# Kernel tuning notes

Measured on AMD Instinct MI355X. Metric: run time of the kernel, lower is better.

The kernel has to match this reference:

```python
import jax, jax.numpy as jnp
import numpy as np

NUM_NODES = 200000
EMB_DIM = 64
NUM_EDGES = 6400000
NUM_LAYERS = 4


def setup_inputs() -> dict:
    key = jax.random.key(0)
    k1, k2, k3, k4 = jax.random.split(key, 4)
    embeds = jax.random.normal(k1, (NUM_NODES, EMB_DIM), dtype=jnp.float32)
    adj_rows = jax.random.randint(k2, (NUM_EDGES,), 0, NUM_NODES, dtype=jnp.int64)
    adj_cols = jax.random.randint(k3, (NUM_EDGES,), 0, NUM_NODES, dtype=jnp.int64)
    adj_vals = jax.random.uniform(k4, (NUM_EDGES,), dtype=jnp.float32)
    return {"embeds": embeds, "adj_rows": adj_rows, "adj_cols": adj_cols, "adj_vals": adj_vals}


def _spmm(rows, cols, vals, x):
    # Sparse (COO) adjacency @ dense x: out[r] += v * x[c]
    msgs = vals[:, None] * x[cols]  # [E, d] gather + scale
    return jax.ops.segment_sum(msgs, rows, num_segments=NUM_NODES)


def reference(embeds, adj_rows, adj_cols, adj_vals):
    x = embeds
    acc = x  # running sum over layer outputs (fuses stack+mean)
    for _ in range(NUM_LAYERS):
        x = _spmm(adj_rows, adj_cols, adj_vals, x)
        acc = acc + x
    return acc / jnp.float32(NUM_LAYERS + 1)
```

## Files before the change

### kernel.cpp

```cpp
#include <hip/hip_runtime.h>

#define N_NODES 200000
#define DIM 64
#define BSHIFT 8
#define BROWS 256
#define NB 782
#define NB_PAD 1024
#define CHUNK 4096
#define NS 8
#define NBINS 2048

__device__ __forceinline__ unsigned short f2bf(float f) {
    unsigned int u = __float_as_uint(f);
    u += 0x7FFFu + ((u >> 16) & 1u);
    return (unsigned short)(u >> 16);
}
__device__ __forceinline__ int stripe_of(int c) { return (int)((unsigned)c / 25000u); }

__global__ __launch_bounds__(256) void bucket_hist(const int* __restrict__ rows, int E,
                                                   int* __restrict__ bcnt) {
    __shared__ int h[NB_PAD];
    for (int i = threadIdx.x; i < NB_PAD; i += 256) h[i] = 0;
    __syncthreads();
    int stride = gridDim.x * blockDim.x;
    for (int e = blockIdx.x * blockDim.x + threadIdx.x; e < E; e += stride)
        atomicAdd(&h[rows[e] >> BSHIFT], 1);
    __syncthreads();
    for (int i = threadIdx.x; i < NB; i += 256)
        if (h[i]) atomicAdd(&bcnt[i], h[i]);
}

__global__ __launch_bounds__(1024) void bucket_scan(const int* __restrict__ bcnt,
                                                    int* __restrict__ bbase,
                                                    int* __restrict__ bcur) {
    __shared__ int wsum[16];
    int t = threadIdx.x;
    int v = (t < NB) ? bcnt[t] : 0;
    int incl = v;
    for (int off = 1; off < 64; off <<= 1) {
        int u = __shfl_up(incl, off);
        if ((t & 63) >= off) incl += u;
    }
    if ((t & 63) == 63) wsum[t >> 6] = incl;
    __syncthreads();
    if (t < 16) {
        int w = wsum[t];
        for (int off = 1; off < 16; off <<= 1) {
            int u = __shfl_up(w, off);
            if (t >= off) w += u;
        }
        wsum[t] = w;
    }
    __syncthreads();
    int wb = (t >= 64) ? wsum[(t >> 6) - 1] : 0;
    int excl = wb + incl - v;
    if (t < NB) { bbase[t] = excl; bcur[t] = excl; }
    if (t == NB - 1) bbase[NB] = excl + v;
}

__global__ __launch_bounds__(512) void bucket_scatter(const int* __restrict__ rows,
                                                      const int* __restrict__ cols,
                                                      const float* __restrict__ vals, int E,
                                                      int* __restrict__ bcur,
                                                      int2* __restrict__ tmp) {
    __shared__ int h[NB_PAD];
    __shared__ int cur2[NB_PAD];
    __shared__ int wtot[8];
    __shared__ int2 stage[CHUNK];
    __shared__ unsigned short sbkt[CHUNK];
    const int base = blockIdx.x * CHUNK;
    const int count = min(CHUNK, E - base);
    const int t = threadIdx.x;

    for (int i = t; i < NB_PAD; i += 512) h[i] = 0;
    __syncthreads();

    int myr[8], myc[8];
    float myv[8];
#pragma unroll
    for (int k = 0; k < 8; ++k) {
        int i = t + k * 512;
        if (i < count) {
            myr[k] = rows[base + i];
            myc[k] = cols[base + i];
            myv[k] = vals[base + i];
            atomicAdd(&h[myr[k] >> BSHIFT], 1);
        }
    }
    __syncthreads();

    int h0 = h[2 * t], h1 = h[2 * t + 1];
    int s = h0 + h1;
    int incl = s;
    for (int off = 1; off < 64; off <<= 1) {
        int u = __shfl_up(incl, off);
        if ((t & 63) >= off) incl += u;
    }
    if ((t & 63) == 63) wtot[t >> 6] = incl;
    __syncthreads();
    int wb = 0;
    for (int w = 0; w < (t >> 6); ++w) wb += wtot[w];
    int excl = wb + incl - s;
    cur2[2 * t] = excl;
    cur2[2 * t + 1] = excl + h0;
    __syncthreads();

    for (int i = t; i < NB; i += 512) {
        int hi = h[i];
        int g = hi ? atomicAdd(&bcur[i], hi) : 0;
        h[i] = g - cur2[i];
    }
    __syncthreads();

#pragma unroll
    for (int k = 0; k < 8; ++k) {
        int i = t + k * 512;
        if (i < count) {
            int r = myr[k];
            int b = r >> BSHIFT;
            int slot = atomicAdd(&cur2[b], 1);
            stage[slot] = make_int2(((r & (BROWS - 1)) << 18) | myc[k], __float_as_int(myv[k]));
            sbkt[slot] = (unsigned short)b;
        }
    }
    __syncthreads();
    for (int s2 = t; s2 < count; s2 += 512)
        tmp[s2 + h[sbkt[s2]]] = stage[s2];
}

__global__ __launch_bounds__(512) void bucket_sort(const int2* __restrict__ tmp,
                                                   const int* __restrict__ bbase,
                                                   int2* __restrict__ sorted,
                                                   int* __restrict__ row_start) {
    __shared__ int h[NBINS];
    __shared__ int wtot[8];
    const int bk = blockIdx.x;
    const int s0 = bbase[bk], s1 = bbase[bk + 1];
    const int t = threadIdx.x;
#pragma unroll
    for (int k = 0; k < NBINS / 512; ++k) h[t + k * 512] = 0;
    __syncthreads();
    for (int e = s0 + t; e < s1; e += 512) {
        int key = tmp[e].x;
        int bin = ((key >> 18) << 3) | stripe_of(key & 0x3FFFF);
        atomicAdd(&h[bin], 1);
    }
    __syncthreads();
    int b[4], ssum = 0;
#pragma unroll
    for (int k = 0; k < 4; ++k) { b[k] = h[4 * t + k]; ssum += b[k]; }
    int incl = ssum;
    for (int off = 1; off < 64; off <<= 1) {
        int u = __shfl_up(incl, off);
        if ((t & 63) >= off) incl += u;
    }
    if ((t & 63) == 63) wtot[t >> 6] = incl;
    __syncthreads();
    int wb = 0;
    for (int w = 0; w < (t >> 6); ++w) wb += wtot[w];
    int run = wb + incl - ssum;
    int rbase = bk << BSHIFT;
#pragma unroll
    for (int k = 0; k < 4; ++k) {
        int bin = 4 * t + k;
        h[bin] = run;
        if ((bin & 7) == 0) {
            int row = rbase + (bin >> 3);
            if (row < N_NODES) row_start[row] = s0 + run;
        }
        run += b[k];
    }
    if (bk == NB - 1 && t == 0) row_start[N_NODES] = s1;
    __syncthreads();
    for (int e = s0 + t; e < s1; e += 512) {
        int2 kv = tmp[e];
        int c = kv.x & 0x3FFFF;
        int bin = ((kv.x >> 18) << 3) | stripe_of(c);
        int rank = atomicAdd(&h[bin], 1);
        sorted[s0 + rank] = make_int2(c, kv.y);
    }
}

__global__ __launch_bounds__(256) void convert_kernel(const float* __restrict__ src,
                                                      unsigned short* __restrict__ dst, int n4) {
    int i = blockIdx.x * blockDim.x + threadIdx.x;
    if (i >= n4) return;
    float4 v = *(const float4*)(src + i * 4);
    ushort4 o;
    o.x = f2bf(v.x); o.y = f2bf(v.y); o.z = f2bf(v.z); o.w = f2bf(v.w);
    *(ushort4*)(dst + i * 4) = o;
}

#define BF_LO(u) __uint_as_float((u) << 16)
#define BF_HI(u) __uint_as_float((u) & 0xFFFF0000u)
#define FMA8(G, V)                              \
    do {                                        \
        a0 = fmaf((V), BF_LO((G).x), a0);       \
        a1 = fmaf((V), BF_HI((G).x), a1);       \
        a2 = fmaf((V), BF_LO((G).y), a2);       \
        a3 = fmaf((V), BF_HI((G).y), a3);       \
        a4 = fmaf((V), BF_LO((G).z), a4);       \
        a5 = fmaf((V), BF_HI((G).z), a5);       \
        a6 = fmaf((V), BF_LO((G).w), a6);       \
        a7 = fmaf((V), BF_HI((G).w), a7);       \
    } while (0)

template <int MODE>
__global__ __launch_bounds__(256) void spmm_kernel(const int2* __restrict__ sorted,
                                                   const int* __restrict__ row_start,
                                                   const unsigned short* __restrict__ xb,
                                                   const float* __restrict__ embeds,
                                                   unsigned short* __restrict__ y,
                                                   float* __restrict__ acc) {
    int gid = blockIdx.x * blockDim.x + threadIdx.x;
    int r = gid >> 3;
    if (r >= N_NODES) return;
    int j = (gid & 7) << 3;
    const unsigned short* xbj = xb + j;
    int e = row_start[r], eend = row_start[r + 1];
    float a0 = 0.f, a1 = 0.f, a2 = 0.f, a3 = 0.f, a4 = 0.f, a5 = 0.f, a6 = 0.f, a7 = 0.f;

    int2 c0 = make_int2(0, 0), c1 = make_int2(0, 0);
    int2 c2 = make_int2(0, 0), c3 = make_int2(0, 0);
    if (e + 4 <= eend) {
        c0 = sorted[e]; c1 = sorted[e + 1]; c2 = sorted[e + 2]; c3 = sorted[e + 3];
    }
    while (e + 8 <= eend) {
        uint4 g0 = *(const uint4*)(xbj + (c0.x << 6));
        uint4 g1 = *(const uint4*)(xbj + (c1.x << 6));
        uint4 g2 = *(const uint4*)(xbj + (c2.x << 6));
        uint4 g3 = *(const uint4*)(xbj + (c3.x << 6));
        int2 n0 = sorted[e + 4], n1 = sorted[e + 5];
        int2 n2 = sorted[e + 6], n3 = sorted[e + 7];
        float v0 = __int_as_float(c0.y), v1 = __int_as_float(c1.y);
        float v2 = __int_as_float(c2.y), v3 = __int_as_float(c3.y);
        FMA8(g0, v0); FMA8(g1, v1); FMA8(g2, v2); FMA8(g3, v3);
        c0 = n0; c1 = n1; c2 = n2; c3 = n3;
        e += 4;
    }
    if (e + 4 <= eend) {
        uint4 g0 = *(const uint4*)(xbj + (c0.x << 6));
        uint4 g1 = *(const uint4*)(xbj + (c1.x << 6));
        uint4 g2 = *(const uint4*)(xbj + (c2.x << 6));
        uint4 g3 = *(const uint4*)(xbj + (c3.x << 6));
        float v0 = __int_as_float(c0.y), v1 = __int_as_float(c1.y);
        float v2 = __int_as_float(c2.y), v3 = __int_as_float(c3.y);
        FMA8(g0, v0); FMA8(g1, v1); FMA8(g2, v2); FMA8(g3, v3);
        e += 4;
    }
    for (; e < eend; ++e) {
        int2 cv = sorted[e];
        uint4 g = *(const uint4*)(xbj + (cv.x << 6));
        float v = __int_as_float(cv.y);
        FMA8(g, v);
    }

    int o = (r << 6) + j;
    if (MODE == 0) {
        uint4 yo;
        yo.x = (unsigned)f2bf(a0) | ((unsigned)f2bf(a1) << 16);
        yo.y = (unsigned)f2bf(a2) | ((unsigned)f2bf(a3) << 16);
        yo.z = (unsigned)f2bf(a4) | ((unsigned)f2bf(a5) << 16);
        yo.w = (unsigned)f2bf(a6) | ((unsigned)f2bf(a7) << 16);
        *(uint4*)(y + o) = yo;
        float4 x0 = *(const float4*)(embeds + o);
        float4 x1 = *(const float4*)(embeds + o + 4);
        *(float4*)(acc + o)     = make_float4(x0.x + a0, x0.y + a1, x0.z + a2, x0.w + a3);
        *(float4*)(acc + o + 4) = make_float4(x1.x + a4, x1.y + a5, x1.z + a6, x1.w + a7);
    } else if (MODE == 1) {
        uint4 yo;
        yo.x = (unsigned)f2bf(a0) | ((unsigned)f2bf(a1) << 16);
        yo.y = (unsigned)f2bf(a2) | ((unsigned)f2bf(a3) << 16);
        yo.z = (unsigned)f2bf(a4) | ((unsigned)f2bf(a5) << 16);
        yo.w = (unsigned)f2bf(a6) | ((unsigned)f2bf(a7) << 16);
        *(uint4*)(y + o) = yo;
        float4 q0 = *(const float4*)(acc + o);
        float4 q1 = *(const float4*)(acc + o + 4);
        *(float4*)(acc + o)     = make_float4(q0.x + a0, q0.y + a1, q0.z + a2, q0.w + a3);
        *(float4*)(acc + o + 4) = make_float4(q1.x + a4, q1.y + a5, q1.z + a6, q1.w + a7);
    } else {
        const float sc = 0.2f;
        float4 q0 = *(const float4*)(acc + o);
        float4 q1 = *(const float4*)(acc + o + 4);
        *(float4*)(acc + o)     = make_float4((q0.x + a0) * sc, (q0.y + a1) * sc,
                                              (q0.z + a2) * sc, (q0.w + a3) * sc);
        *(float4*)(acc + o + 4) = make_float4((q1.x + a4) * sc, (q1.y + a5) * sc,
                                              (q1.z + a6) * sc, (q1.w + a7) * sc);
    }
}

extern "C" void kernel_launch(void* const* d_in, const int* in_sizes, int n_in,
                              void* d_out, int out_size, void* d_ws, size_t ws_size,
                              hipStream_t stream) {
    const float* embeds = (const float*)d_in[0];
    const int*   rows   = (const int*)d_in[1];
    const int*   cols   = (const int*)d_in[2];
    const float* vals   = (const float*)d_in[3];
    float* acc = (float*)d_out;
    const int E = in_sizes[1];

    char* ws = (char*)d_ws;
    size_t off = 0;
    auto alloc = [&](size_t bytes) -> char* {
        char* p = ws + off;
        off = (off + bytes + 255) & ~(size_t)255;
        return p;
    };
    int*   bcnt      = (int*)alloc((size_t)NB * 4);
    int*   bbase     = (int*)alloc((size_t)(NB + 1) * 4);
    int*   bcur      = (int*)alloc((size_t)NB * 4);
    int*   row_start = (int*)alloc((size_t)(N_NODES + 1) * 4);
    int2*  sorted    = (int2*)alloc((size_t)E * 8);
    unsigned short* xb0 = (unsigned short*)alloc((size_t)N_NODES * DIM * 2);
    unsigned short* xb1 = (unsigned short*)alloc((size_t)N_NODES * DIM * 2);
    int2*  tmp       = (int2*)alloc((size_t)E * 8);

    hipMemsetAsync(bcnt, 0, (size_t)NB * 4, stream);

    bucket_hist<<<1024, 256, 0, stream>>>(rows, E, bcnt);
    bucket_scan<<<1, 1024, 0, stream>>>(bcnt, bbase, bcur);
    bucket_scatter<<<(E + CHUNK - 1) / CHUNK, 512, 0, stream>>>(rows, cols, vals, E, bcur, tmp);
    bucket_sort<<<NB, 512, 0, stream>>>(tmp, bbase, sorted, row_start);

    int n4 = N_NODES * DIM / 4;
    convert_kernel<<<(n4 + 255) / 256, 256, 0, stream>>>(embeds, xb0, n4);

    int sb = (N_NODES * 8 + 255) / 256;
    spmm_kernel<0><<<sb, 256, 0, stream>>>(sorted, row_start, xb0, embeds, xb1, acc);
    spmm_kernel<1><<<sb, 256, 0, stream>>>(sorted, row_start, xb1, embeds, xb0, acc);
    spmm_kernel<1><<<sb, 256, 0, stream>>>(sorted, row_start, xb0, embeds, xb1, acc);
    spmm_kernel<2><<<sb, 256, 0, stream>>>(sorted, row_start, xb1, embeds, xb0, acc);
}
```

Before: 850.8 us.

## Stripe-ordered per-bucket SpMM with deferred layer merge kernel

The bucket sort now orders edges stripe-major within each 256-row bucket and writes per-stripe row offsets. The SpMM becomes one block per bucket that walks the column stripes in turn, with each thread accumulating 8 rows, so gathered x rows are reused while a stripe is hot in cache. The per-layer fp32 accumulator read-modify-write is replaced by keeping all four layer outputs in bf16 and combining them in a single final merge kernel. The cost is far fewer, register-heavy threads with only two gathers in flight each, which may hurt latency hiding. The edge stream is read with nontemporal loads, and the temp sort buffer is reused as storage for two layer outputs.

```diff
diff --git a/kernel.cpp b/kernel.cpp
--- a/kernel.cpp
+++ b/kernel.cpp
@@ -9,7 +9,11 @@
 #define CHUNK 4096
 #define NS 8
 #define NBINS 2048
-
+#define RS2_PITCH 257
+
+__device__ __forceinline__ float bf2f(unsigned short u) {
+    return __uint_as_float(((unsigned int)u) << 16);
+}
 __device__ __forceinline__ unsigned short f2bf(float f) {
     unsigned int u = __float_as_uint(f);
     u += 0x7FFFu + ((u >> 16) & 1u);
@@ -131,7 +135,7 @@
 __global__ __launch_bounds__(512) void bucket_sort(const int2* __restrict__ tmp,
                                                    const int* __restrict__ bbase,
                                                    int2* __restrict__ sorted,
-                                                   int* __restrict__ row_start) {
+                                                   int* __restrict__ rs2) {
     __shared__ int h[NBINS];
     __shared__ int wtot[8];
     const int bk = blockIdx.x;
@@ -142,7 +146,7 @@
     __syncthreads();
     for (int e = s0 + t; e < s1; e += 512) {
         int key = tmp[e].x;
-        int bin = ((key >> 18) << 3) | stripe_of(key & 0x3FFFF);
+        int bin = (stripe_of(key & 0x3FFFF) << 8) | (key >> 18);
         atomicAdd(&h[bin], 1);
     }
     __syncthreads();
@@ -159,23 +163,22 @@
     int wb = 0;
     for (int w = 0; w < (t >> 6); ++w) wb += wtot[w];
     int run = wb + incl - ssum;
-    int rbase = bk << BSHIFT;
-#pragma unroll
-    for (int k = 0; k < 4; ++k) {
-        int bin = 4 * t + k;
-        h[bin] = run;
-        if ((bin & 7) == 0) {
-            int row = rbase + (bin >> 3);
-            if (row < N_NODES) row_start[row] = s0 + run;
-        }
-        run += b[k];
-    }
-    if (bk == NB - 1 && t == 0) row_start[N_NODES] = s1;
+#pragma unroll
+    for (int k = 0; k < 4; ++k) { h[4 * t + k] = run; run += b[k]; }
+    __syncthreads();
+    for (int i = t; i < NS * RS2_PITCH; i += 512) {
+        int s = i / RS2_PITCH;
+        int rl = i - s * RS2_PITCH;
+        int val;
+        if (rl < 256) val = s0 + h[(s << 8) + rl];
+        else          val = (s < NS - 1) ? s0 + h[(s + 1) << 8] : s1;
+        rs2[((size_t)s * NB + bk) * RS2_PITCH + rl] = val;
+    }
     __syncthreads();
     for (int e = s0 + t; e < s1; e += 512) {
         int2 kv = tmp[e];
         int c = kv.x & 0x3FFFF;
-        int bin = ((kv.x >> 18) << 3) | stripe_of(c);
+        int bin = (stripe_of(c) << 8) | (kv.x >> 18);
         int rank = atomicAdd(&h[bin], 1);
         sorted[s0 + rank] = make_int2(c, kv.y);
     }
@@ -193,100 +196,110 @@
 
 #define BF_LO(u) __uint_as_float((u) << 16)
 #define BF_HI(u) __uint_as_float((u) & 0xFFFF0000u)
-#define FMA8(G, V)                              \
+#define FMA8A(A, G, V)                          \
     do {                                        \
-        a0 = fmaf((V), BF_LO((G).x), a0);       \
-        a1 = fmaf((V), BF_HI((G).x), a1);       \
-        a2 = fmaf((V), BF_LO((G).y), a2);       \
-        a3 = fmaf((V), BF_HI((G).y), a3);       \
-        a4 = fmaf((V), BF_LO((G).z), a4);       \
-        a5 = fmaf((V), BF_HI((G).z), a5);       \
-        a6 = fmaf((V), BF_LO((G).w), a6);       \
-        a7 = fmaf((V), BF_HI((G).w), a7);       \
+        A[0] = fmaf((V), BF_LO((G).x), A[0]);   \
+        A[1] = fmaf((V), BF_HI((G).x), A[1]);   \
+        A[2] = fmaf((V), BF_LO((G).y), A[2]);   \
+        A[3] = fmaf((V), BF_HI((G).y), A[3]);   \
+        A[4] = fmaf((V), BF_LO((G).z), A[4]);   \
+        A[5] = fmaf((V), BF_HI((G).z), A[5]);   \
+        A[6] = fmaf((V), BF_LO((G).w), A[6]);   \
+        A[7] = fmaf((V), BF_HI((G).w), A[7]);   \
     } while (0)
 
-template <int MODE>
-__global__ __launch_bounds__(256) void spmm_kernel(const int2* __restrict__ sorted,
-                                                   const int* __restrict__ row_start,
-                                                   const unsigned short* __restrict__ xb,
-                                                   const float* __restrict__ embeds,
-                                                   unsigned short* __restrict__ y,
-                                                   float* __restrict__ acc) {
-    int gid = blockIdx.x * blockDim.x + threadIdx.x;
-    int r = gid >> 3;
-    if (r >= N_NODES) return;
-    int j = (gid & 7) << 3;
+__global__ __launch_bounds__(256, 4) void spmm_kernel(const int2* __restrict__ sorted,
+                                                      const int* __restrict__ rs2,
+                                                      const unsigned short* __restrict__ xb,
+                                                      unsigned short* __restrict__ y) {
+    __shared__ int rsl[NS * RS2_PITCH];
+    const int bk = blockIdx.x;
+    const int t = threadIdx.x;
+    for (int i = t; i < NS * RS2_PITCH; i += 256) {
+        int s = i / RS2_PITCH;
+        rsl[i] = rs2[((size_t)s * NB + bk) * RS2_PITCH + (i - s * RS2_PITCH)];
+    }
+    __syncthreads();
+
+    const int j = (t & 7) << 3;
+    const int rl0 = t >> 3;
     const unsigned short* xbj = xb + j;
-    int e = row_start[r], eend = row_start[r + 1];
-    float a0 = 0.f, a1 = 0.f, a2 = 0.f, a3 = 0.f, a4 = 0.f, a5 = 0.f, a6 = 0.f, a7 = 0.f;
-
-    int2 c0 = make_int2(0, 0), c1 = make_int2(0, 0);
-    int2 c2 = make_int2(0, 0), c3 = make_int2(0, 0);
-    if (e + 4 <= eend) {
-        c0 = sorted[e]; c1 = sorted[e + 1]; c2 = sorted[e + 2]; c3 = sorted[e + 3];
-    }
-    while (e + 8 <= eend) {
-        uint4 g0 = *(const uint4*)(xbj + (c0.x << 6));
-        uint4 g1 = *(const uint4*)(xbj + (c1.x << 6));
-        uint4 g2 = *(const uint4*)(xbj + (c2.x << 6));
-        uint4 g3 = *(const uint4*)(xbj + (c3.x << 6));
-        int2 n0 = sorted[e + 4], n1 = sorted[e + 5];
-        int2 n2 = sorted[e + 6], n3 = sorted[e + 7];
-        float v0 = __int_as_float(c0.y), v1 = __int_as_float(c1.y);
-        float v2 = __int_as_float(c2.y), v3 = __int_as_float(c3.y);
-        FMA8(g0, v0); FMA8(g1, v1); FMA8(g2, v2); FMA8(g3, v3);
-        c0 = n0; c1 = n1; c2 = n2; c3 = n3;
-        e += 4;
-    }
-    if (e + 4 <= eend) {
-        uint4 g0 = *(const uint4*)(xbj + (c0.x << 6));
-        uint4 g1 = *(const uint4*)(xbj + (c1.x << 6));
-        uint4 g2 = *(const uint4*)(xbj + (c2.x << 6));
-        uint4 g3 = *(const uint4*)(xbj + (c3.x << 6));
-        float v0 = __int_as_float(c0.y), v1 = __int_as_float(c1.y);
-        float v2 = __int_as_float(c2.y), v3 = __int_as_float(c3.y);
-        FMA8(g0, v0); FMA8(g1, v1); FMA8(g2, v2); FMA8(g3, v3);
-        e += 4;
-    }
-    for (; e < eend; ++e) {
-        int2 cv = sorted[e];
-        uint4 g = *(const uint4*)(xbj + (cv.x << 6));
-        float v = __int_as_float(cv.y);
-        FMA8(g, v);
-    }
-
-    int o = (r << 6) + j;
-    if (MODE == 0) {
-        uint4 yo;
-        yo.x = (unsigned)f2bf(a0) | ((unsigned)f2bf(a1) << 16);
-        yo.y = (unsigned)f2bf(a2) | ((unsigned)f2bf(a3) << 16);
-        yo.z = (unsigned)f2bf(a4) | ((unsigned)f2bf(a5) << 16);
-        yo.w = (unsigned)f2bf(a6) | ((unsigned)f2bf(a7) << 16);
-        *(uint4*)(y + o) = yo;
-        float4 x0 = *(const float4*)(embeds + o);
-        float4 x1 = *(const float4*)(embeds + o + 4);
-        *(float4*)(acc + o)     = make_float4(x0.x + a0, x0.y + a1, x0.z + a2, x0.w + a3);
-        *(float4*)(acc + o + 4) = make_float4(x1.x + a4, x1.y + a5, x1.z + a6, x1.w + a7);
-    } else if (MODE == 1) {
-        uint4 yo;
-        yo.x = (unsigned)f2bf(a0) | ((unsigned)f2bf(a1) << 16);
-        yo.y = (unsigned)f2bf(a2) | ((unsigned)f2bf(a3) << 16);
-        yo.z = (unsigned)f2bf(a4) | ((unsigned)f2bf(a5) << 16);
-        yo.w = (unsigned)f2bf(a6) | ((unsigned)f2bf(a7) << 16);
-        *(uint4*)(y + o) = yo;
-        float4 q0 = *(const float4*)(acc + o);
-        float4 q1 = *(const float4*)(acc + o + 4);
-        *(float4*)(acc + o)     = make_float4(q0.x + a0, q0.y + a1, q0.z + a2, q0.w + a3);
-        *(float4*)(acc + o + 4) = make_float4(q1.x + a4, q1.y + a5, q1.z + a6, q1.w + a7);
-    } else {
-        const float sc = 0.2f;
-        float4 q0 = *(const float4*)(acc + o);
-        float4 q1 = *(const float4*)(acc + o + 4);
-        *(float4*)(acc + o)     = make_float4((q0.x + a0) * sc, (q0.y + a1) * sc,
-                                              (q0.z + a2) * sc, (q0.w + a3) * sc);
-        *(float4*)(acc + o + 4) = make_float4((q1.x + a4) * sc, (q1.y + a5) * sc,
-                                              (q1.z + a6) * sc, (q1.w + a7) * sc);
-    }
+    float acc_[8][8];
+#pragma unroll
+    for (int k = 0; k < 8; ++k)
+#pragma unroll
+        for (int i = 0; i < 8; ++i) acc_[k][i] = 0.f;
+
+#pragma unroll
+    for (int s = 0; s < NS; ++s) {
+#pragma unroll
+        for (int k = 0; k < 8; ++k) {
+            int rl = (rl0 << 3) + k;
+            int e = rsl[s * RS2_PITCH + rl];
+            int eend = rsl[s * RS2_PITCH + rl + 1];
+            for (; e + 2 <= eend; e += 2) {
+                long long r0 = __builtin_nontemporal_load((const long long*)(sorted + e));
+                long long r1 = __builtin_nontemporal_load((const long long*)(sorted + e + 1));
+                int c0 = (int)(unsigned int)r0;
+                int c1 = (int)(unsigned int)r1;
+                float v0 = __int_as_float((int)((unsigned long long)r0 >> 32));
+                float v1 = __int_as_float((int)((unsigned long long)r1 >> 32));
+                uint4 g0 = *(const uint4*)(xbj + (c0 << 6));
+                uint4 g1 = *(const uint4*)(xbj + (c1 << 6));
+                FMA8A(acc_[k], g0, v0);
+                FMA8A(acc_[k], g1, v1);
+            }
+            if (e < eend) {
+                long long r0 = __builtin_nontemporal_load((const long long*)(sorted + e));
+                int c0 = (int)(unsigned int)r0;
+                float v0 = __int_as_float((int)((unsigned long long)r0 >> 32));
+                uint4 g0 = *(const uint4*)(xbj + (c0 << 6));
+                FMA8A(acc_[k], g0, v0);
+            }
+        }
+    }
+
+#pragma unroll
+    for (int k = 0; k < 8; ++k) {
+        int r = (bk << 8) + (rl0 << 3) + k;
+        if (r < N_NODES) {
+            uint4 yo;
+            yo.x = (unsigned)f2bf(acc_[k][0]) | ((unsigned)f2bf(acc_[k][1]) << 16);
+            yo.y = (unsigned)f2bf(acc_[k][2]) | ((unsigned)f2bf(acc_[k][3]) << 16);
+            yo.z = (unsigned)f2bf(acc_[k][4]) | ((unsigned)f2bf(acc_[k][5]) << 16);
+            yo.w = (unsigned)f2bf(acc_[k][6]) | ((unsigned)f2bf(acc_[k][7]) << 16);
+            *(uint4*)(y + (r << 6) + j) = yo;
+        }
+    }
+}
+
+__global__ __launch_bounds__(256) void merge_kernel(const float* __restrict__ emb,
+                                                    const unsigned short* __restrict__ y1,
+                                                    const unsigned short* __restrict__ y2,
+                                                    const unsigned short* __restrict__ y3,
+                                                    const unsigned short* __restrict__ y4,
+                                                    float* __restrict__ acc, int n8) {
+    int i = blockIdx.x * blockDim.x + threadIdx.x;
+    if (i >= n8) return;
+    int o = i * 8;
+    uint4 a = *(const uint4*)(y1 + o);
+    uint4 b = *(const uint4*)(y2 + o);
+    uint4 c = *(const uint4*)(y3 + o);
+    uint4 d = *(const uint4*)(y4 + o);
+    float4 x0 = *(const float4*)(emb + o);
+    float4 x1 = *(const float4*)(emb + o + 4);
+    const float sc = 0.2f;
+    float4 o0, o1;
+    o0.x = (x0.x + BF_LO(a.x) + BF_LO(b.x) + BF_LO(c.x) + BF_LO(d.x)) * sc;
+    o0.y = (x0.y + BF_HI(a.x) + BF_HI(b.x) + BF_HI(c.x) + BF_HI(d.x)) * sc;
+    o0.z = (x0.z + BF_LO(a.y) + BF_LO(b.y) + BF_LO(c.y) + BF_LO(d.y)) * sc;
+    o0.w = (x0.w + BF_HI(a.y) + BF_HI(b.y) + BF_HI(c.y) + BF_HI(d.y)) * sc;
+    o1.x = (x1.x + BF_LO(a.z) + BF_LO(b.z) + BF_LO(c.z) + BF_LO(d.z)) * sc;
+    o1.y = (x1.y + BF_HI(a.z) + BF_HI(b.z) + BF_HI(c.z) + BF_HI(d.z)) * sc;
+    o1.z = (x1.z + BF_LO(a.w) + BF_LO(b.w) + BF_LO(c.w) + BF_LO(d.w)) * sc;
+    o1.w = (x1.w + BF_HI(a.w) + BF_HI(b.w) + BF_HI(c.w) + BF_HI(d.w)) * sc;
+    *(float4*)(acc + o) = o0;
+    *(float4*)(acc + o + 4) = o1;
 }
 
 extern "C" void kernel_launch(void* const* d_in, const int* in_sizes, int n_in,
@@ -306,28 +319,33 @@
         off = (off + bytes + 255) & ~(size_t)255;
         return p;
     };
-    int*   bcnt      = (int*)alloc((size_t)NB * 4);
-    int*   bbase     = (int*)alloc((size_t)(NB + 1) * 4);
-    int*   bcur      = (int*)alloc((size_t)NB * 4);
-    int*   row_start = (int*)alloc((size_t)(N_NODES + 1) * 4);
-    int2*  sorted    = (int2*)alloc((size_t)E * 8);
+    int*   bcnt   = (int*)alloc((size_t)NB * 4);
+    int*   bbase  = (int*)alloc((size_t)(NB + 1) * 4);
+    int*   bcur   = (int*)alloc((size_t)NB * 4);
+    int*   rs2    = (int*)alloc((size_t)NS * NB * RS2_PITCH * 4);
+    int2*  sorted = (int2*)alloc((size_t)E * 8);
     unsigned short* xb0 = (unsigned short*)alloc((size_t)N_NODES * DIM * 2);
     unsigned short* xb1 = (unsigned short*)alloc((size_t)N_NODES * DIM * 2);
-    int2*  tmp       = (int2*)alloc((size_t)E * 8);
+    unsigned short* xb2 = (unsigned short*)alloc((size_t)N_NODES * DIM * 2);
+    int2*  tmp    = (int2*)alloc((size_t)E * 8);
+    unsigned short* xb3 = (unsigned short*)tmp;
+    unsigned short* xb4 = xb3 + (size_t)N_NODES * DIM;
 
     hipMemsetAsync(bcnt, 0, (size_t)NB * 4, stream);
 
     bucket_hist<<<1024, 256, 0, stream>>>(rows, E, bcnt);
     bucket_scan<<<1, 1024, 0, stream>>>(bcnt, bbase, bcur);
     bucket_scatter<<<(E + CHUNK - 1) / CHUNK, 512, 0, stream>>>(rows, cols, vals, E, bcur, tmp);
-    bucket_sort<<<NB, 512, 0, stream>>>(tmp, bbase, sorted, row_start);
+    bucket_sort<<<NB, 512, 0, stream>>>(tmp, bbase, sorted, rs2);
 
     int n4 = N_NODES * DIM / 4;
     convert_kernel<<<(n4 + 255) / 256, 256, 0, stream>>>(embeds, xb0, n4);
 
-    int sb = (N_NODES * 8 + 255) / 256;
-    spmm_kernel<0><<<sb, 256, 0, stream>>>(sorted, row_start, xb0, embeds, xb1, acc);
-    spmm_kernel<1><<<sb, 256, 0, stream>>>(sorted, row_start, xb1, embeds, xb0, acc);
-    spmm_kernel<1><<<sb, 256, 0, stream>>>(sorted, row_start, xb0, embeds, xb1, acc);
-    spmm_kernel<2><<<sb, 256, 0, stream>>>(sorted, row_start, xb1, embeds, xb0, acc);
-}
+    spmm_kernel<<<NB, 256, 0, stream>>>(sorted, rs2, xb0, xb1);
+    spmm_kernel<<<NB, 256, 0, stream>>>(sorted, rs2, xb1, xb2);
+    spmm_kernel<<<NB, 256, 0, stream>>>(sorted, rs2, xb2, xb3);
+    spmm_kernel<<<NB, 256, 0, stream>>>(sorted, rs2, xb3, xb4);
+
+    int n8 = N_NODES * DIM / 8;
+    merge_kernel<<<(n8 + 255) / 256, 256, 0, stream>>>(embeds, xb1, xb2, xb3, xb4, acc, n8);
+}
```

Measured after the change: 1.404 ms. 65.0% more time.
